# Kernel optimization log

Measured on AMD Instinct MI355X. Metric: run time of the kernel, lower is better.

## Reference

```python
import jax, jax.numpy as jnp
import numpy as np

B, NPIX, M, N_CP, N_CA = 8, 256, 8192, 24576, 24576
EPS = 1e-16


def setup_inputs() -> dict:
    key = jax.random.key(0)
    k1, k2, k3, k4, k5, k6 = jax.random.split(key, 6)
    images = jax.random.normal(k1, (B, NPIX, NPIX), dtype=jnp.float32)
    # k-space trajectory in radians/pixel, range [-pi, pi) as torchkbnufft expects
    ktraj = (jax.random.uniform(k2, (2, M), dtype=jnp.float32) * 2.0 - 1.0) * np.float32(np.pi)
    pulsefac = jax.random.normal(k3, (2, M), dtype=jnp.float32)
    cphase_sign = jnp.sign(jax.random.normal(k4, (3, N_CP), dtype=jnp.float32))
    cphase_ind = jax.random.randint(k5, (3, N_CP), 0, M, dtype=jnp.int32)
    camp_ind = jax.random.randint(k6, (4, N_CA), 0, M, dtype=jnp.int32)
    return {"images": images, "ktraj": ktraj, "pulsefac": pulsefac,
            "cphase_sign": cphase_sign, "cphase_ind": cphase_ind, "camp_ind": camp_ind}


def reference(images, ktraj, pulsefac, cphase_sign, cphase_ind, camp_ind):
    npix = images.shape[-1]
    # centered image coordinates (Fessler NUFFT convention, n_shift = npix//2)
    coords = (jnp.arange(npix) - npix // 2).astype(jnp.float32)
    kv, ku = ktraj[0], ktraj[1]  # (M,) each
    # separable exact NDFT: exp(-i(kv*y + ku*x)) = Ev[m,y] * Eu[m,x]
    Ev = jnp.exp(-1j * kv[:, None] * coords[None, :]).astype(jnp.complex64)  # (M, npix)
    Eu = jnp.exp(-1j * ku[:, None] * coords[None, :]).astype(jnp.complex64)  # (M, npix)
    img_c = images.astype(jnp.complex64)
    tmp = jnp.einsum('byx,my->bmx', img_c, Ev)        # (B, M, npix)
    kdata = jnp.einsum('bmx,mx->bm', tmp, Eu)          # (B, M) complex visibilities
    # pulse-function correction (complex multiply)
    pf = pulsefac[0] + 1j * pulsefac[1]                # (M,)
    vis_c = kdata * pf                                 # (B, M)
    vis = jnp.stack([vis_c.real, vis_c.imag], axis=1)  # (B, 2, M)
    visamp = jnp.sqrt(vis_c.real ** 2 + vis_c.imag ** 2 + EPS)  # (B, M)
    # closure phases: gather triangle visibilities, signed phase sum, degrees
    v_tri = vis_c[:, cphase_ind]                       # (B, 3, N_cp)
    ang = jnp.arctan2(v_tri.imag, v_tri.real)          # (B, 3, N_cp)
    cphase = jnp.einsum('kn,bkn->bn', cphase_sign, ang) * np.float32(180.0 / np.pi)
    # log closure amplitudes: gather quadrangle visibilities
    v_quad = vis_c[:, camp_ind]                        # (B, 4, N_ca)
    amp = jnp.sqrt(v_quad.real ** 2 + v_quad.imag ** 2 + EPS)
    logcamp = (jnp.log(amp[:, 0]) + jnp.log(amp[:, 1])
               - jnp.log(amp[:, 2]) - jnp.log(amp[:, 3]))  # (B, N_ca)
    return vis, visamp, cphase, logcamp
```

## Files before the change

### kernel.cpp

```cpp
#include <hip/hip_runtime.h>
#include <cmath>

#define BB   8
#define NPIX 256
#define MM   8192
#define NCP  24576
#define NCA  24576
#define EPSF 1e-16f

#define KC   32
#define KCW  40
#define TMB  64

#define VIS_OFF    0
#define VISAMP_OFF (BB * 2 * MM)
#define CPH_OFF    (VISAMP_OFF + BB * MM)
#define LCA_OFF    (CPH_OFF + BB * NCP)

typedef __bf16 bf16x8 __attribute__((ext_vector_type(8)));
typedef float  f32x4  __attribute__((ext_vector_type(4)));

__global__ __launch_bounds__(256, 2)
void nufft_vis_mfma(const float* __restrict__ images,
                    const float* __restrict__ ktraj,
                    const float* __restrict__ pulsefac,
                    float* __restrict__ out)
{
    __shared__ __align__(16) __bf16 sA_hi[128 * KCW];
    __shared__ __align__(16) __bf16 sA_lo[128 * KCW];
    __shared__ __align__(16) __bf16 sB_hi[NPIX * KCW];
    __shared__ __align__(16) __bf16 sB_lo[NPIX * KCW];

    const int tid  = threadIdx.x;
    const int m0   = blockIdx.x * TMB;
    const int b    = blockIdx.y;
    const int lane = tid & 63;
    const int w    = tid >> 6;
    const int ln15 = lane & 15;
    const int q    = lane >> 4;

    const int am  = tid >> 2;
    const int ajg = tid & 3;
    const float kvm = ktraj[m0 + am];
    float rots, rotc;
    sincosf(kvm, &rots, &rotc);
    const float* imgb = images + b * NPIX * NPIX + tid;

    f32x4 acc[2][16];
    #pragma unroll
    for (int rt = 0; rt < 2; ++rt)
        #pragma unroll
        for (int ct = 0; ct < 16; ++ct)
            acc[rt][ct] = (f32x4){0.f, 0.f, 0.f, 0.f};

    for (int y0 = 0; y0 < NPIX; y0 += KC) {
        {
            float s, c;
            sincosf(kvm * (float)(y0 + ajg * 8 - 128), &s, &c);
            float er = c, ei = -s;
            bf16x8 vrh, vrl, vih, vil;
            #pragma unroll
            for (int j = 0; j < 8; ++j) {
                __bf16 h = (__bf16)er;
                vrh[j] = h; vrl[j] = (__bf16)(er - (float)h);
                h = (__bf16)ei;
                vih[j] = h; vil[j] = (__bf16)(ei - (float)h);
                const float nr = er * rotc + ei * rots;
                const float ni = ei * rotc - er * rots;
                er = nr; ei = ni;
            }
            *(bf16x8*)&sA_hi[am * KCW + ajg * 8]        = vrh;
            *(bf16x8*)&sA_lo[am * KCW + ajg * 8]        = vrl;
            *(bf16x8*)&sA_hi[(64 + am) * KCW + ajg * 8] = vih;
            *(bf16x8*)&sA_lo[(64 + am) * KCW + ajg * 8] = vil;
        }
        #pragma unroll
        for (int g = 0; g < 4; ++g) {
            bf16x8 bh, bl;
            #pragma unroll
            for (int j = 0; j < 8; ++j) {
                const float v = imgb[(y0 + g * 8 + j) * NPIX];
                const __bf16 h = (__bf16)v;
                bh[j] = h; bl[j] = (__bf16)(v - (float)h);
            }
            *(bf16x8*)&sB_hi[tid * KCW + g * 8] = bh;
            *(bf16x8*)&sB_lo[tid * KCW + g * 8] = bl;
        }
        __syncthreads();

        bf16x8 a_h[2], a_l[2];
        const int ar0 = w * 16 + ln15;
        a_h[0] = *(const bf16x8*)&sA_hi[ar0 * KCW + q * 8];
        a_l[0] = *(const bf16x8*)&sA_lo[ar0 * KCW + q * 8];
        a_h[1] = *(const bf16x8*)&sA_hi[(64 + ar0) * KCW + q * 8];
        a_l[1] = *(const bf16x8*)&sA_lo[(64 + ar0) * KCW + q * 8];

        #pragma unroll
        for (int ct = 0; ct < 16; ++ct) {
            const int brow = ct * 16 + ln15;
            const bf16x8 bh = *(const bf16x8*)&sB_hi[brow * KCW + q * 8];
            const bf16x8 bl = *(const bf16x8*)&sB_lo[brow * KCW + q * 8];
            #pragma unroll
            for (int rt = 0; rt < 2; ++rt) {
                acc[rt][ct] = __builtin_amdgcn_mfma_f32_16x16x32_bf16(a_h[rt], bh, acc[rt][ct], 0, 0, 0);
                acc[rt][ct] = __builtin_amdgcn_mfma_f32_16x16x32_bf16(a_h[rt], bl, acc[rt][ct], 0, 0, 0);
                acc[rt][ct] = __builtin_amdgcn_mfma_f32_16x16x32_bf16(a_l[rt], bh, acc[rt][ct], 0, 0, 0);
            }
        }
        __syncthreads();
    }

    #pragma unroll
    for (int r = 0; r < 4; ++r) {
        const int m = m0 + w * 16 + q * 4 + r;
        const float ku = ktraj[MM + m];
        float s0, c0, s16, c16;
        sincosf(ku * (float)(ln15 - 128), &s0, &c0);
        sincosf(ku * 16.0f, &s16, &c16);
        float er = c0, ei = -s0;
        float sr = 0.f, si = 0.f;
        #pragma unroll
        for (int ct = 0; ct < 16; ++ct) {
            const float tr = acc[0][ct][r];
            const float ti = acc[1][ct][r];
            sr = fmaf(tr, er, fmaf(-ti, ei, sr));
            si = fmaf(tr, ei, fmaf(ti, er, si));
            const float nr = er * c16 + ei * s16;
            const float ni = ei * c16 - er * s16;
            er = nr; ei = ni;
        }
        #pragma unroll
        for (int off = 8; off >= 1; off >>= 1) {
            sr += __shfl_xor(sr, off);
            si += __shfl_xor(si, off);
        }
        if (ln15 == 0) {
            const float pr = pulsefac[m];
            const float pi = pulsefac[MM + m];
            const float vr = sr * pr - si * pi;
            const float vi = sr * pi + si * pr;
            out[b * 2 * MM + m]      = vr;
            out[b * 2 * MM + MM + m] = vi;
            out[VISAMP_OFF + b * MM + m] = sqrtf(vr * vr + vi * vi + EPSF);
        }
    }
}

__global__ void cphase_kernel(const float* __restrict__ vis,
                              const float* __restrict__ sign,
                              const int* __restrict__ ind,
                              float* __restrict__ out)
{
    const int i = blockIdx.x * blockDim.x + threadIdx.x;
    if (i >= BB * NCP) return;
    const int b = i / NCP;
    const int n = i - b * NCP;
    float acc = 0.f;
    #pragma unroll
    for (int k = 0; k < 3; ++k) {
        const int m = ind[k * NCP + n];
        const float vr = vis[b * 2 * MM + m];
        const float vi = vis[b * 2 * MM + MM + m];
        acc += sign[k * NCP + n] * atan2f(vi, vr);
    }
    out[CPH_OFF + i] = acc * 57.295779513082323f;
}

__global__ void logcamp_kernel(const float* __restrict__ vis,
                               const int* __restrict__ ind,
                               float* __restrict__ out)
{
    const int i = blockIdx.x * blockDim.x + threadIdx.x;
    if (i >= BB * NCA) return;
    const int b = i / NCA;
    const int n = i - b * NCA;
    float acc = 0.f;
    #pragma unroll
    for (int k = 0; k < 4; ++k) {
        const int m = ind[k * NCA + n];
        const float vr = vis[b * 2 * MM + m];
        const float vi = vis[b * 2 * MM + MM + m];
        const float a = sqrtf(vr * vr + vi * vi + EPSF);
        acc += (k < 2 ? 1.f : -1.f) * logf(a);
    }
    out[LCA_OFF + i] = acc;
}

extern "C" void kernel_launch(void* const* d_in, const int* in_sizes, int n_in,
                              void* d_out, int out_size, void* d_ws, size_t ws_size,
                              hipStream_t stream)
{
    const float* images   = (const float*)d_in[0];
    const float* ktraj    = (const float*)d_in[1];
    const float* pulsefac = (const float*)d_in[2];
    const float* csign    = (const float*)d_in[3];
    const int*   cind     = (const int*)d_in[4];
    const int*   caind    = (const int*)d_in[5];
    float* out = (float*)d_out;

    dim3 grid(MM / TMB, BB);
    nufft_vis_mfma<<<grid, 256, 0, stream>>>(images, ktraj, pulsefac, out);
    cphase_kernel<<<(BB * NCP + 255) / 256, 256, 0, stream>>>(out, csign, cind, out);
    logcamp_kernel<<<(BB * NCA + 255) / 256, 256, 0, stream>>>(out, caind, out);
}
```

Before: 125.5 us.

## Swizzle LDS tiles into MFMA-fragment layout, raise occupancy, fuse gather kernels

Replaces the padded row-major LDS tiles (stride 40) with a fragment-ordered layout in which each 16-row group stores its k8 slices contiguously. This shrinks shared memory and aims for conflict-free 16-byte reads. Launch bounds go from 2 to 3 blocks per SM, and the two post-processing kernels (closure phase and log closure amplitude) become one launch. The log of sqrt is rewritten as 0.5*log of the squared magnitude. The higher occupancy target may force register spills given the large accumulator array.

```diff
diff --git a/kernel.cpp b/kernel.cpp
--- a/kernel.cpp
+++ b/kernel.cpp
@@ -9,7 +9,6 @@
 #define EPSF 1e-16f
 
 #define KC   32
-#define KCW  40
 #define TMB  64
 
 #define VIS_OFF    0
@@ -20,16 +19,20 @@
 typedef __bf16 bf16x8 __attribute__((ext_vector_type(8)));
 typedef float  f32x4  __attribute__((ext_vector_type(4)));
 
-__global__ __launch_bounds__(256, 2)
+#define WIDX(row, k8) (((row) >> 4) * 512 + (k8) * 128 + ((row) & 15) * 8)
+
+__global__ __launch_bounds__(256, 3)
 void nufft_vis_mfma(const float* __restrict__ images,
                     const float* __restrict__ ktraj,
                     const float* __restrict__ pulsefac,
                     float* __restrict__ out)
 {
-    __shared__ __align__(16) __bf16 sA_hi[128 * KCW];
-    __shared__ __align__(16) __bf16 sA_lo[128 * KCW];
-    __shared__ __align__(16) __bf16 sB_hi[NPIX * KCW];
-    __shared__ __align__(16) __bf16 sB_lo[NPIX * KCW];
+    __shared__ __align__(16) __bf16 sArh[TMB * KC];
+    __shared__ __align__(16) __bf16 sArl[TMB * KC];
+    __shared__ __align__(16) __bf16 sAih[TMB * KC];
+    __shared__ __align__(16) __bf16 sAil[TMB * KC];
+    __shared__ __align__(16) __bf16 sBh[NPIX * KC];
+    __shared__ __align__(16) __bf16 sBl[NPIX * KC];
 
     const int tid  = threadIdx.x;
     const int m0   = blockIdx.x * TMB;
@@ -69,43 +72,45 @@
                 const float ni = ei * rotc - er * rots;
                 er = nr; ei = ni;
             }
-            *(bf16x8*)&sA_hi[am * KCW + ajg * 8]        = vrh;
-            *(bf16x8*)&sA_lo[am * KCW + ajg * 8]        = vrl;
-            *(bf16x8*)&sA_hi[(64 + am) * KCW + ajg * 8] = vih;
-            *(bf16x8*)&sA_lo[(64 + am) * KCW + ajg * 8] = vil;
-        }
-        #pragma unroll
-        for (int g = 0; g < 4; ++g) {
+            const int ao = WIDX(am, ajg);
+            *(bf16x8*)&sArh[ao] = vrh;
+            *(bf16x8*)&sArl[ao] = vrl;
+            *(bf16x8*)&sAih[ao] = vih;
+            *(bf16x8*)&sAil[ao] = vil;
+        }
+        #pragma unroll
+        for (int gg = 0; gg < 4; ++gg) {
             bf16x8 bh, bl;
             #pragma unroll
             for (int j = 0; j < 8; ++j) {
-                const float v = imgb[(y0 + g * 8 + j) * NPIX];
+                const float v = imgb[(y0 + gg * 8 + j) * NPIX];
                 const __bf16 h = (__bf16)v;
                 bh[j] = h; bl[j] = (__bf16)(v - (float)h);
             }
-            *(bf16x8*)&sB_hi[tid * KCW + g * 8] = bh;
-            *(bf16x8*)&sB_lo[tid * KCW + g * 8] = bl;
+            const int bo = WIDX(tid, gg);
+            *(bf16x8*)&sBh[bo] = bh;
+            *(bf16x8*)&sBl[bo] = bl;
         }
         __syncthreads();
 
-        bf16x8 a_h[2], a_l[2];
-        const int ar0 = w * 16 + ln15;
-        a_h[0] = *(const bf16x8*)&sA_hi[ar0 * KCW + q * 8];
-        a_l[0] = *(const bf16x8*)&sA_lo[ar0 * KCW + q * 8];
-        a_h[1] = *(const bf16x8*)&sA_hi[(64 + ar0) * KCW + q * 8];
-        a_l[1] = *(const bf16x8*)&sA_lo[(64 + ar0) * KCW + q * 8];
+        const int ar = w * 16 + ln15;
+        const int aro = WIDX(ar, q);
+        const bf16x8 ah0 = *(const bf16x8*)&sArh[aro];
+        const bf16x8 al0 = *(const bf16x8*)&sArl[aro];
+        const bf16x8 ah1 = *(const bf16x8*)&sAih[aro];
+        const bf16x8 al1 = *(const bf16x8*)&sAil[aro];
 
         #pragma unroll
         for (int ct = 0; ct < 16; ++ct) {
-            const int brow = ct * 16 + ln15;
-            const bf16x8 bh = *(const bf16x8*)&sB_hi[brow * KCW + q * 8];
-            const bf16x8 bl = *(const bf16x8*)&sB_lo[brow * KCW + q * 8];
-            #pragma unroll
-            for (int rt = 0; rt < 2; ++rt) {
-                acc[rt][ct] = __builtin_amdgcn_mfma_f32_16x16x32_bf16(a_h[rt], bh, acc[rt][ct], 0, 0, 0);
-                acc[rt][ct] = __builtin_amdgcn_mfma_f32_16x16x32_bf16(a_h[rt], bl, acc[rt][ct], 0, 0, 0);
-                acc[rt][ct] = __builtin_amdgcn_mfma_f32_16x16x32_bf16(a_l[rt], bh, acc[rt][ct], 0, 0, 0);
-            }
+            const int bro = WIDX(ct * 16 + ln15, q);
+            const bf16x8 bh = *(const bf16x8*)&sBh[bro];
+            const bf16x8 bl = *(const bf16x8*)&sBl[bro];
+            acc[0][ct] = __builtin_amdgcn_mfma_f32_16x16x32_bf16(ah0, bh, acc[0][ct], 0, 0, 0);
+            acc[0][ct] = __builtin_amdgcn_mfma_f32_16x16x32_bf16(ah0, bl, acc[0][ct], 0, 0, 0);
+            acc[0][ct] = __builtin_amdgcn_mfma_f32_16x16x32_bf16(al0, bh, acc[0][ct], 0, 0, 0);
+            acc[1][ct] = __builtin_amdgcn_mfma_f32_16x16x32_bf16(ah1, bh, acc[1][ct], 0, 0, 0);
+            acc[1][ct] = __builtin_amdgcn_mfma_f32_16x16x32_bf16(ah1, bl, acc[1][ct], 0, 0, 0);
+            acc[1][ct] = __builtin_amdgcn_mfma_f32_16x16x32_bf16(al1, bh, acc[1][ct], 0, 0, 0);
         }
         __syncthreads();
     }
@@ -146,44 +151,36 @@
     }
 }
 
-__global__ void cphase_kernel(const float* __restrict__ vis,
-                              const float* __restrict__ sign,
-                              const int* __restrict__ ind,
-                              float* __restrict__ out)
+__global__ void gather_fused(const float* __restrict__ vis,
+                             const float* __restrict__ sign,
+                             const int* __restrict__ cind,
+                             const int* __restrict__ caind,
+                             float* __restrict__ out)
 {
-    const int i = blockIdx.x * blockDim.x + threadIdx.x;
+    const int i = blockIdx.x * 256 + threadIdx.x;
     if (i >= BB * NCP) return;
     const int b = i / NCP;
     const int n = i - b * NCP;
-    float acc = 0.f;
+    const float* vb = vis + b * 2 * MM;
+
+    float cp = 0.f;
     #pragma unroll
     for (int k = 0; k < 3; ++k) {
-        const int m = ind[k * NCP + n];
-        const float vr = vis[b * 2 * MM + m];
-        const float vi = vis[b * 2 * MM + MM + m];
-        acc += sign[k * NCP + n] * atan2f(vi, vr);
-    }
-    out[CPH_OFF + i] = acc * 57.295779513082323f;
-}
-
-__global__ void logcamp_kernel(const float* __restrict__ vis,
-                               const int* __restrict__ ind,
-                               float* __restrict__ out)
-{
-    const int i = blockIdx.x * blockDim.x + threadIdx.x;
-    if (i >= BB * NCA) return;
-    const int b = i / NCA;
-    const int n = i - b * NCA;
-    float acc = 0.f;
+        const int m = cind[k * NCP + n];
+        cp += sign[k * NCP + n] * atan2f(vb[MM + m], vb[m]);
+    }
+    out[CPH_OFF + i] = cp * 57.29577951308232f;
+
+    float lc = 0.f;
     #pragma unroll
     for (int k = 0; k < 4; ++k) {
-        const int m = ind[k * NCA + n];
-        const float vr = vis[b * 2 * MM + m];
-        const float vi = vis[b * 2 * MM + MM + m];
-        const float a = sqrtf(vr * vr + vi * vi + EPSF);
-        acc += (k < 2 ? 1.f : -1.f) * logf(a);
-    }
-    out[LCA_OFF + i] = acc;
+        const int m = caind[k * NCA + n];
+        const float vr = vb[m];
+        const float vi = vb[MM + m];
+        const float l = 0.5f * logf(vr * vr + vi * vi + EPSF);
+        lc += (k < 2) ? l : -l;
+    }
+    out[LCA_OFF + i] = lc;
 }
 
 extern "C" void kernel_launch(void* const* d_in, const int* in_sizes, int n_in,
@@ -200,6 +197,5 @@
 
     dim3 grid(MM / TMB, BB);
     nufft_vis_mfma<<<grid, 256, 0, stream>>>(images, ktraj, pulsefac, out);
-    cphase_kernel<<<(BB * NCP + 255) / 256, 256, 0, stream>>>(out, csign, cind, out);
-    logcamp_kernel<<<(BB * NCA + 255) / 256, 256, 0, stream>>>(out, caind, out);
+    gather_fused<<<(BB * NCP + 255) / 256, 256, 0, stream>>>(out, csign, cind, caind, out);
 }
```

Result: slower. 167.1 us (+33.1%).
